# Kernel tuning notes

Measured on AMD Instinct MI355X. Metric: run time of the kernel, lower is better.

The kernel has to match this reference:

```python
import jax, jax.numpy as jnp
import numpy as np

B, T = 64, 2000
Q_DIM, MEM_DIM, ATT_DIM = 1024, 512, 128
N_FILTERS, KERNEL = 32, 31


def setup_inputs() -> dict:
    key = jax.random.key(0)
    ks = jax.random.split(key, 8)
    s = lambda fan_in: 1.0 / np.sqrt(fan_in)
    return {
        "attention_hidden_state": jax.random.normal(ks[0], (B, Q_DIM), jnp.float32),
        "memory": jax.random.normal(ks[1], (B, T, MEM_DIM), jnp.float32),
        "attention_weights_cat": jax.random.uniform(ks[2], (B, 2, T), jnp.float32),
        "W_query": jax.random.normal(ks[3], (Q_DIM, ATT_DIM), jnp.float32) * s(Q_DIM),
        "W_memory": jax.random.normal(ks[4], (MEM_DIM, ATT_DIM), jnp.float32) * s(MEM_DIM),
        "W_v": jax.random.normal(ks[5], (ATT_DIM, 1), jnp.float32) * s(ATT_DIM),
        "W_conv": jax.random.normal(ks[6], (KERNEL, 2, N_FILTERS), jnp.float32) * s(KERNEL * 2),  # WIO layout
        "W_loc": jax.random.normal(ks[7], (N_FILTERS, ATT_DIM), jnp.float32) * s(N_FILTERS),
    }


def reference(attention_hidden_state, memory, attention_weights_cat,
              W_query, W_memory, W_v, W_conv, W_loc):
    # processed query: [B, 1, D]
    pq = jnp.tanh(attention_hidden_state @ W_query)[:, None, :]
    # processed memory: [B, T, D]
    pm = jnp.tanh(jnp.einsum('btm,md->btd', memory, W_memory))
    # location features: Conv1D 'same', no bias, channels-last input [B, T, 2]
    awc = jnp.transpose(attention_weights_cat, (0, 2, 1))
    conv = jax.lax.conv_general_dilated(
        awc, W_conv, window_strides=(1,), padding='SAME',
        dimension_numbers=('NWC', 'WIO', 'NWC'))  # [B, T, F]
    ploc = jnp.tanh(conv @ W_loc)  # [B, T, D]
    # energies: [B, T]
    energies = jnp.squeeze(jnp.tanh(pq + ploc + pm) @ W_v, -1)
    attention_weights = jax.nn.softmax(energies, axis=1)  # [B, T]
    attention_context = jnp.einsum('bt,btm->bm', attention_weights, memory)
    return attention_context, attention_weights
```

## Files before the change

kernel.cpp:

```cpp
#include <hip/hip_runtime.h>
#include <hip/hip_bf16.h>

typedef __attribute__((ext_vector_type(8))) short s16x8;
typedef __attribute__((ext_vector_type(4))) float f32x4;

#define B_SZ 64
#define T_SZ 2000
#define QD 1024
#define MD 512
#define AD 128
#define NF 32
#define KW 31
#define TT 64
#define NT2 32
#define ASTRIDE 1056

__device__ __forceinline__ unsigned short f2bf(float f) {
    unsigned int u = __float_as_uint(f);
    unsigned int r = (u + 0x7FFFu + ((u >> 16) & 1u)) >> 16;
    return (unsigned short)r;
}
__device__ __forceinline__ unsigned int pack2bf_manual(float a, float b) {
    return (unsigned int)f2bf(a) | ((unsigned int)f2bf(b) << 16);
}
__device__ __forceinline__ unsigned int pack2bf(float a, float b) {
    union { __hip_bfloat162 h; unsigned int u; } cv;
    cv.h = __float22bfloat162_rn(float2{a, b});
    return cv.u;
}
__device__ __forceinline__ float fast_tanh(float x) {
    float ax = fabsf(x);
    float e = __expf(2.0f * ax);
    float r = 1.0f - 2.0f * __builtin_amdgcn_rcpf(e + 1.0f);
    return x < 0.0f ? -r : r;
}

__global__ __launch_bounds__(256) void prep_kernel(
    const float* __restrict__ ahs, const float* __restrict__ Wq,
    const float* __restrict__ Wm, const float* __restrict__ Wl,
    float* __restrict__ pq, unsigned short* __restrict__ WB,
    unsigned short* __restrict__ WL) {
    const int blk = blockIdx.x, tid = threadIdx.x;
    if (blk < 64) {
        __shared__ float q_sm[QD];
        __shared__ float part[AD];
        ((float4*)q_sm)[tid] = ((const float4*)(ahs + blk * QD))[tid];
        __syncthreads();
        const int d = tid & 127, kh = tid >> 7;
        const int k0 = kh * 512;
        float a0 = 0, a1 = 0, a2 = 0, a3 = 0;
        for (int k = k0; k < k0 + 512; k += 4) {
            a0 += q_sm[k]     * Wq[(k)     * AD + d];
            a1 += q_sm[k + 1] * Wq[(k + 1) * AD + d];
            a2 += q_sm[k + 2] * Wq[(k + 2) * AD + d];
            a3 += q_sm[k + 3] * Wq[(k + 3) * AD + d];
        }
        float s = (a0 + a1) + (a2 + a3);
        if (kh) part[d] = s;
        __syncthreads();
        if (tid < AD) pq[blk * AD + tid] = fast_tanh(s + part[tid]);
    } else if (blk < 96) {
        int cidx = (blk - 64) * 256 + tid;
        int n = cidx >> 10, s = (cidx >> 6) & 15, l = cidx & 63;
        int col = n * 16 + (l & 15);
        int krow = s * 32 + (l >> 4) * 8;
        float v[8];
        #pragma unroll
        for (int j = 0; j < 8; ++j) v[j] = Wm[(krow + j) * AD + col];
        uint4 pk;
        pk.x = pack2bf(v[0], v[1]); pk.y = pack2bf(v[2], v[3]);
        pk.z = pack2bf(v[4], v[5]); pk.w = pack2bf(v[6], v[7]);
        *(uint4*)(WB + cidx * 8) = pk;
    } else {
        for (int h = 0; h < 2; ++h) {
            int cidx = h * 256 + tid;
            int n = cidx >> 6, l = cidx & 63;
            int col = n * 16 + (l & 15);
            int krow = (l >> 4) * 8;
            float v[8];
            #pragma unroll
            for (int j = 0; j < 8; ++j) v[j] = Wl[(krow + j) * AD + col];
            uint4 pk;
            pk.x = pack2bf_manual(v[0], v[1]); pk.y = pack2bf_manual(v[2], v[3]);
            pk.z = pack2bf_manual(v[4], v[5]); pk.w = pack2bf_manual(v[6], v[7]);
            *(uint4*)(WL + cidx * 8) = pk;
        }
    }
}

__global__ __launch_bounds__(512, 4) void energy_kernel(
    const float* __restrict__ memory, const float* __restrict__ awcat,
    const float* __restrict__ Wconv, const float* __restrict__ Wv,
    const float* __restrict__ pq, const unsigned short* __restrict__ WB,
    const unsigned short* __restrict__ WL, float* __restrict__ wts,
    float* __restrict__ ctile, float* __restrict__ mloc,
    float* __restrict__ Stile) {
    const int tile = blockIdx.x;
    const int b = blockIdx.y;
    const int t0 = tile * TT;
    const int tid = threadIdx.x;

    __shared__ __align__(16) unsigned short Atile[TT * (ASTRIDE / 2)];
    __shared__ float aw_sm[2][96];
    __shared__ __align__(16) unsigned short conv_sm[TT * 40];
    __shared__ float e_part[TT][8];
    __shared__ float e_sm[TT];
    __shared__ float p_sm[TT];
    __shared__ float cpart[2][MD];

    if (tid < 192) {
        int c = tid / 96, i = tid % 96;
        float v = 0.0f;
        int tv = t0 - 15 + i;
        if (i < 94 && tv >= 0 && tv < T_SZ) v = awcat[(b * 2 + c) * T_SZ + tv];
        aw_sm[c][i] = v;
    }

    {
        const float4* msrc = (const float4*)(memory + ((size_t)b * T_SZ + t0) * MD);
        #pragma unroll
        for (int it = 0; it < 8; ++it) {
            int cid = it * 512 + tid;
            int r = cid >> 6, cc = cid & 63;
            float4 v0 = {0, 0, 0, 0}, v1 = {0, 0, 0, 0};
            if (t0 + r < T_SZ) {
                v0 = msrc[r * 128 + cc * 2];
                v1 = msrc[r * 128 + cc * 2 + 1];
            }
            uint4 pk;
            pk.x = pack2bf(v0.x, v0.y); pk.y = pack2bf(v0.z, v0.w);
            pk.z = pack2bf(v1.x, v1.y); pk.w = pack2bf(v1.z, v1.w);
            int off = r * ASTRIDE + ((cc * 16) ^ ((r & 7) << 4));
            *(uint4*)((char*)Atile + off) = pk;
        }
    }
    __syncthreads();

    {
        int f = tid & 31, tq = tid >> 5;
        float acc[4] = {0, 0, 0, 0};
        for (int k = 0; k < KW; ++k) {
            #pragma unroll
            for (int c = 0; c < 2; ++c) {
                float wv = Wconv[(k * 2 + c) * NF + f];
                #pragma unroll
                for (int tt = 0; tt < 4; ++tt)
                    acc[tt] += wv * aw_sm[c][tq + tt * 16 + k];
            }
        }
        #pragma unroll
        for (int tt = 0; tt < 4; ++tt)
            conv_sm[(tq + tt * 16) * 40 + f] = f2bf(acc[tt]);
    }
    __syncthreads();

    const int w = tid >> 6, l = tid & 63;
    const int lr = l & 15, lg = l >> 4;
    const int d = w * 16 + lr;
    const float pqv = pq[b * AD + d];
    const float wvv = Wv[d];

    f32x4 zero4 = {0, 0, 0, 0};
    f32x4 acc[4] = {zero4, zero4, zero4, zero4};

    const s16x8* wbp = (const s16x8*)WB;
    const int swz = (lr & 7) << 4;
    const char* Ac = (const char*)Atile;

    #pragma unroll
    for (int s = 0; s < 16; ++s) {
        s16x8 bf = wbp[(w * 16 + s) * 64 + l];
        int j = (lg * 16 + s * 64) ^ swz;
        #pragma unroll
        for (int rt = 0; rt < 4; ++rt) {
            s16x8 a = *(const s16x8*)(Ac + (rt * 16 + lr) * ASTRIDE + j);
            acc[rt] = __builtin_amdgcn_mfma_f32_16x16x32_bf16(a, bf, acc[rt], 0, 0, 0);
        }
    }

    const s16x8* wlp = (const s16x8*)WL;
    s16x8 lb = wlp[w * 64 + l];
    f32x4 q[4];
    #pragma unroll
    for (int rt = 0; rt < 4; ++rt) {
        s16x8 la = *(const s16x8*)((const char*)conv_sm + ((rt * 16 + lr) * 80 + lg * 16));
        q[rt] = __builtin_amdgcn_mfma_f32_16x16x32_bf16(la, lb, zero4, 0, 0, 0);
    }

    #pragma unroll
    for (int rt = 0; rt < 4; ++rt) {
        #pragma unroll
        for (int r = 0; r < 4; ++r) {
            float v = fast_tanh(pqv + fast_tanh(q[rt][r]) + fast_tanh(acc[rt][r])) * wvv;
            v += __shfl_xor(v, 1);
            v += __shfl_xor(v, 2);
            v += __shfl_xor(v, 4);
            v += __shfl_xor(v, 8);
            if (lr == 0) e_part[rt * 16 + lg * 4 + r][w] = v;
        }
    }
    __syncthreads();

    {
        int t = tid >> 3, g = tid & 7;
        float v = e_part[t][g];
        v += __shfl_xor(v, 1);
        v += __shfl_xor(v, 2);
        v += __shfl_xor(v, 4);
        if (g == 0) e_sm[t] = (t0 + t < T_SZ) ? v : -3.4e38f;
    }
    __syncthreads();

    if (tid < TT) {
        float e = e_sm[tid];
        float m = e;
        m = fmaxf(m, __shfl_xor(m, 1));  m = fmaxf(m, __shfl_xor(m, 2));
        m = fmaxf(m, __shfl_xor(m, 4));  m = fmaxf(m, __shfl_xor(m, 8));
        m = fmaxf(m, __shfl_xor(m, 16)); m = fmaxf(m, __shfl_xor(m, 32));
        bool valid = (t0 + tid < T_SZ);
        float p = valid ? __expf(e - m) : 0.0f;
        p_sm[tid] = p;
        float S = p;
        S += __shfl_xor(S, 1);  S += __shfl_xor(S, 2);
        S += __shfl_xor(S, 4);  S += __shfl_xor(S, 8);
        S += __shfl_xor(S, 16); S += __shfl_xor(S, 32);
        if (valid) wts[b * T_SZ + t0 + tid] = p;
        if (tid == 0) { mloc[b * NT2 + tile] = m; Stile[b * NT2 + tile] = S; }
    }
    __syncthreads();

    {
        int grp = tid >> 8, idx = tid & 255;
        int boff = idx * 4;
        float c0 = 0.0f, c1 = 0.0f;
        #pragma unroll
        for (int tt = 0; tt < 32; ++tt) {
            int t = grp * 32 + tt;
            float p = p_sm[t];
            unsigned int pk = *(const unsigned int*)(
                Ac + t * ASTRIDE + (boff ^ ((t & 7) << 4)));
            c0 += p * __uint_as_float(pk << 16);
            c1 += p * __uint_as_float(pk & 0xffff0000u);
        }
        cpart[grp][idx * 2]     = c0;
        cpart[grp][idx * 2 + 1] = c1;
    }
    __syncthreads();
    ctile[((b * NT2 + tile) << 9) + tid] = cpart[0][tid] + cpart[1][tid];
}

__global__ __launch_bounds__(256) void finalize_kernel(
    const float* __restrict__ mloc, const float* __restrict__ Stile,
    const float* __restrict__ ctile, float* __restrict__ wts,
    float* __restrict__ ctx) {
    const int b = blockIdx.x, h = blockIdx.y, tid = threadIdx.x;
    __shared__ float sc_sm[NT2];
    if (tid < 64) {
        float m = (tid < NT2) ? mloc[b * NT2 + tid] : -3.4e38f;
        float s = (tid < NT2) ? Stile[b * NT2 + tid] : 0.0f;
        float M = m;
        M = fmaxf(M, __shfl_xor(M, 1));  M = fmaxf(M, __shfl_xor(M, 2));
        M = fmaxf(M, __shfl_xor(M, 4));  M = fmaxf(M, __shfl_xor(M, 8));
        M = fmaxf(M, __shfl_xor(M, 16)); M = fmaxf(M, __shfl_xor(M, 32));
        float e = __expf(m - M);
        float z = e * s;
        z += __shfl_xor(z, 1);  z += __shfl_xor(z, 2);
        z += __shfl_xor(z, 4);  z += __shfl_xor(z, 8);
        z += __shfl_xor(z, 16); z += __shfl_xor(z, 32);
        if (tid < NT2) sc_sm[tid] = e / z;
    }
    __syncthreads();

    if (h == 0) {
        #pragma unroll
        for (int i = 0; i < 8; ++i) {
            int idx = tid + i * 256;
            if (idx < T_SZ) wts[b * T_SZ + idx] *= sc_sm[idx >> 6];
        }
    }

    float a = 0.0f;
    const float* cb = ctile + ((size_t)b * NT2 << 9) + h * 256 + tid;
    #pragma unroll 8
    for (int tl = 0; tl < NT2; ++tl) a += sc_sm[tl] * cb[tl << 9];
    ctx[b * MD + h * 256 + tid] = a;
}

extern "C" void kernel_launch(void* const* d_in, const int* in_sizes, int n_in,
                              void* d_out, int out_size, void* d_ws, size_t ws_size,
                              hipStream_t stream) {
    const float* ahs    = (const float*)d_in[0];
    const float* memory = (const float*)d_in[1];
    const float* awcat  = (const float*)d_in[2];
    const float* Wq     = (const float*)d_in[3];
    const float* Wm     = (const float*)d_in[4];
    const float* Wv     = (const float*)d_in[5];
    const float* Wconv  = (const float*)d_in[6];
    const float* Wl     = (const float*)d_in[7];

    float* out = (float*)d_out;
    float* ctx = out;
    float* wts = out + B_SZ * MD;

    char* ws = (char*)d_ws;
    float* pq             = (float*)(ws);
    unsigned short* WB    = (unsigned short*)(ws + 32768);
    unsigned short* WL    = (unsigned short*)(ws + 163840);
    float* mloc           = (float*)(ws + 172032);
    float* Stile          = (float*)(ws + 180224);
    float* ctile          = (float*)(ws + 196608);

    prep_kernel<<<97, 256, 0, stream>>>(ahs, Wq, Wm, Wl, pq, WB, WL);
    energy_kernel<<<dim3(NT2, B_SZ), 512, 0, stream>>>(
        memory, awcat, Wconv, Wv, pq, WB, WL, wts, ctile, mloc, Stile);
    finalize_kernel<<<dim3(B_SZ, 2), 256, 0, stream>>>(mloc, Stile, ctile, wts, ctx);
}
```

Measured before the change: 100.3 us.

## Halve energy tile to 32 timesteps with 2x2 MFMA register blocking per wave

```diff
diff --git a/kernel.cpp b/kernel.cpp
--- a/kernel.cpp
+++ b/kernel.cpp
@@ -11,8 +11,7 @@
 #define AD 128
 #define NF 32
 #define KW 31
-#define TT 64
-#define NT2 32
+#define NTILE 63
 #define ASTRIDE 1056
 
 __device__ __forceinline__ unsigned short f2bf(float f) {
@@ -35,7 +34,7 @@
     return x < 0.0f ? -r : r;
 }
 
-__global__ __launch_bounds__(256) void prep_kernel(
+__global__ __launch_bounds__(512) void prep_kernel(
     const float* __restrict__ ahs, const float* __restrict__ Wq,
     const float* __restrict__ Wm, const float* __restrict__ Wl,
     float* __restrict__ pq, unsigned short* __restrict__ WB,
@@ -43,24 +42,27 @@
     const int blk = blockIdx.x, tid = threadIdx.x;
     if (blk < 64) {
         __shared__ float q_sm[QD];
-        __shared__ float part[AD];
-        ((float4*)q_sm)[tid] = ((const float4*)(ahs + blk * QD))[tid];
+        __shared__ float part[3][AD];
+        ((float2*)q_sm)[tid] = ((const float2*)(ahs + blk * QD))[tid];
         __syncthreads();
         const int d = tid & 127, kh = tid >> 7;
-        const int k0 = kh * 512;
+        const int k0 = kh * 256;
         float a0 = 0, a1 = 0, a2 = 0, a3 = 0;
-        for (int k = k0; k < k0 + 512; k += 4) {
+        #pragma unroll 4
+        for (int k = k0; k < k0 + 256; k += 4) {
             a0 += q_sm[k]     * Wq[(k)     * AD + d];
             a1 += q_sm[k + 1] * Wq[(k + 1) * AD + d];
             a2 += q_sm[k + 2] * Wq[(k + 2) * AD + d];
             a3 += q_sm[k + 3] * Wq[(k + 3) * AD + d];
         }
         float s = (a0 + a1) + (a2 + a3);
-        if (kh) part[d] = s;
+        if (kh) part[kh - 1][d] = s;
         __syncthreads();
-        if (tid < AD) pq[blk * AD + tid] = fast_tanh(s + part[tid]);
-    } else if (blk < 96) {
-        int cidx = (blk - 64) * 256 + tid;
+        if (tid < AD)
+            pq[blk * AD + tid] =
+                fast_tanh((s + part[0][tid]) + (part[1][tid] + part[2][tid]));
+    } else if (blk < 80) {
+        int cidx = (blk - 64) * 512 + tid;
         int n = cidx >> 10, s = (cidx >> 6) & 15, l = cidx & 63;
         int col = n * 16 + (l & 15);
         int krow = s * 32 + (l >> 4) * 8;
@@ -72,23 +74,21 @@
         pk.z = pack2bf(v[4], v[5]); pk.w = pack2bf(v[6], v[7]);
         *(uint4*)(WB + cidx * 8) = pk;
     } else {
-        for (int h = 0; h < 2; ++h) {
-            int cidx = h * 256 + tid;
-            int n = cidx >> 6, l = cidx & 63;
-            int col = n * 16 + (l & 15);
-            int krow = (l >> 4) * 8;
-            float v[8];
-            #pragma unroll
-            for (int j = 0; j < 8; ++j) v[j] = Wl[(krow + j) * AD + col];
-            uint4 pk;
-            pk.x = pack2bf_manual(v[0], v[1]); pk.y = pack2bf_manual(v[2], v[3]);
-            pk.z = pack2bf_manual(v[4], v[5]); pk.w = pack2bf_manual(v[6], v[7]);
-            *(uint4*)(WL + cidx * 8) = pk;
-        }
-    }
-}
-
-__global__ __launch_bounds__(512, 4) void energy_kernel(
+        int cidx = tid;
+        int n = cidx >> 6, l = cidx & 63;
+        int col = n * 16 + (l & 15);
+        int krow = (l >> 4) * 8;
+        float v[8];
+        #pragma unroll
+        for (int j = 0; j < 8; ++j) v[j] = Wl[(krow + j) * AD + col];
+        uint4 pk;
+        pk.x = pack2bf_manual(v[0], v[1]); pk.y = pack2bf_manual(v[2], v[3]);
+        pk.z = pack2bf_manual(v[4], v[5]); pk.w = pack2bf_manual(v[6], v[7]);
+        *(uint4*)(WL + cidx * 8) = pk;
+    }
+}
+
+__global__ __launch_bounds__(256) void energy_kernel(
     const float* __restrict__ memory, const float* __restrict__ awcat,
     const float* __restrict__ Wconv, const float* __restrict__ Wv,
     const float* __restrict__ pq, const unsigned short* __restrict__ WB,
@@ -97,22 +97,20 @@
     float* __restrict__ Stile) {
     const int tile = blockIdx.x;
     const int b = blockIdx.y;
-    const int t0 = tile * TT;
+    const int t0 = tile * 32;
     const int tid = threadIdx.x;
 
-    __shared__ __align__(16) unsigned short Atile[TT * (ASTRIDE / 2)];
-    __shared__ float aw_sm[2][96];
-    __shared__ __align__(16) unsigned short conv_sm[TT * 40];
-    __shared__ float e_part[TT][8];
-    __shared__ float e_sm[TT];
-    __shared__ float p_sm[TT];
-    __shared__ float cpart[2][MD];
-
-    if (tid < 192) {
-        int c = tid / 96, i = tid % 96;
+    __shared__ __align__(16) unsigned short Atile[32 * (ASTRIDE / 2)];
+    __shared__ float aw_sm[2][64];
+    __shared__ __align__(16) unsigned short conv_sm[32 * 40];
+    __shared__ float e_part[32][4];
+    __shared__ float p_sm[32];
+
+    if (tid < 128) {
+        int c = tid >> 6, i = tid & 63;
         float v = 0.0f;
         int tv = t0 - 15 + i;
-        if (i < 94 && tv >= 0 && tv < T_SZ) v = awcat[(b * 2 + c) * T_SZ + tv];
+        if (i < 63 && tv >= 0 && tv < T_SZ) v = awcat[(b * 2 + c) * T_SZ + tv];
         aw_sm[c][i] = v;
     }
 
@@ -120,7 +118,7 @@
         const float4* msrc = (const float4*)(memory + ((size_t)b * T_SZ + t0) * MD);
         #pragma unroll
         for (int it = 0; it < 8; ++it) {
-            int cid = it * 512 + tid;
+            int cid = it * 256 + tid;
             int r = cid >> 6, cc = cid & 63;
             float4 v0 = {0, 0, 0, 0}, v1 = {0, 0, 0, 0};
             if (t0 + r < T_SZ) {
@@ -145,108 +143,110 @@
                 float wv = Wconv[(k * 2 + c) * NF + f];
                 #pragma unroll
                 for (int tt = 0; tt < 4; ++tt)
-                    acc[tt] += wv * aw_sm[c][tq + tt * 16 + k];
+                    acc[tt] += wv * aw_sm[c][tq + tt * 8 + k];
             }
         }
         #pragma unroll
         for (int tt = 0; tt < 4; ++tt)
-            conv_sm[(tq + tt * 16) * 40 + f] = f2bf(acc[tt]);
+            conv_sm[(tq + tt * 8) * 40 + f] = f2bf(acc[tt]);
     }
     __syncthreads();
 
     const int w = tid >> 6, l = tid & 63;
     const int lr = l & 15, lg = l >> 4;
-    const int d = w * 16 + lr;
-    const float pqv = pq[b * AD + d];
-    const float wvv = Wv[d];
+    const int d0 = (2 * w + 0) * 16 + lr;
+    const int d1 = (2 * w + 1) * 16 + lr;
+    const float pqv0 = pq[b * AD + d0], pqv1 = pq[b * AD + d1];
+    const float wvv0 = Wv[d0], wvv1 = Wv[d1];
 
     f32x4 zero4 = {0, 0, 0, 0};
-    f32x4 acc[4] = {zero4, zero4, zero4, zero4};
+    f32x4 p00 = zero4, p01 = zero4, p10 = zero4, p11 = zero4;
 
     const s16x8* wbp = (const s16x8*)WB;
     const int swz = (lr & 7) << 4;
-    const char* Ac = (const char*)Atile;
+    const int rbase0 = lr * ASTRIDE;
+    const int rbase1 = (16 + lr) * ASTRIDE;
+    const int inb = lg * 16;
 
     #pragma unroll
     for (int s = 0; s < 16; ++s) {
-        s16x8 bf = wbp[(w * 16 + s) * 64 + l];
-        int j = (lg * 16 + s * 64) ^ swz;
-        #pragma unroll
-        for (int rt = 0; rt < 4; ++rt) {
-            s16x8 a = *(const s16x8*)(Ac + (rt * 16 + lr) * ASTRIDE + j);
-            acc[rt] = __builtin_amdgcn_mfma_f32_16x16x32_bf16(a, bf, acc[rt], 0, 0, 0);
-        }
-    }
-
+        int j = (inb + s * 64) ^ swz;
+        s16x8 a0 = *(const s16x8*)((const char*)Atile + rbase0 + j);
+        s16x8 a1 = *(const s16x8*)((const char*)Atile + rbase1 + j);
+        s16x8 b0 = wbp[((2 * w + 0) * 16 + s) * 64 + l];
+        s16x8 b1 = wbp[((2 * w + 1) * 16 + s) * 64 + l];
+        p00 = __builtin_amdgcn_mfma_f32_16x16x32_bf16(a0, b0, p00, 0, 0, 0);
+        p01 = __builtin_amdgcn_mfma_f32_16x16x32_bf16(a0, b1, p01, 0, 0, 0);
+        p10 = __builtin_amdgcn_mfma_f32_16x16x32_bf16(a1, b0, p10, 0, 0, 0);
+        p11 = __builtin_amdgcn_mfma_f32_16x16x32_bf16(a1, b1, p11, 0, 0, 0);
+    }
+
+    s16x8 la0 = *(const s16x8*)((const char*)conv_sm + (lr * 80 + lg * 16));
+    s16x8 la1 = *(const s16x8*)((const char*)conv_sm + ((16 + lr) * 80 + lg * 16));
     const s16x8* wlp = (const s16x8*)WL;
-    s16x8 lb = wlp[w * 64 + l];
-    f32x4 q[4];
+    s16x8 lb0 = wlp[(2 * w + 0) * 64 + l];
+    s16x8 lb1 = wlp[(2 * w + 1) * 64 + l];
+    f32x4 q00 = __builtin_amdgcn_mfma_f32_16x16x32_bf16(la0, lb0, zero4, 0, 0, 0);
+    f32x4 q01 = __builtin_amdgcn_mfma_f32_16x16x32_bf16(la0, lb1, zero4, 0, 0, 0);
+    f32x4 q10 = __builtin_amdgcn_mfma_f32_16x16x32_bf16(la1, lb0, zero4, 0, 0, 0);
+    f32x4 q11 = __builtin_amdgcn_mfma_f32_16x16x32_bf16(la1, lb1, zero4, 0, 0, 0);
+
+    float vr[8];
     #pragma unroll
-    for (int rt = 0; rt < 4; ++rt) {
-        s16x8 la = *(const s16x8*)((const char*)conv_sm + ((rt * 16 + lr) * 80 + lg * 16));
-        q[rt] = __builtin_amdgcn_mfma_f32_16x16x32_bf16(la, lb, zero4, 0, 0, 0);
-    }
-
+    for (int r = 0; r < 4; ++r) {
+        vr[r]     = fast_tanh(pqv0 + fast_tanh(q00[r]) + fast_tanh(p00[r])) * wvv0
+                  + fast_tanh(pqv1 + fast_tanh(q01[r]) + fast_tanh(p01[r])) * wvv1;
+        vr[4 + r] = fast_tanh(pqv0 + fast_tanh(q10[r]) + fast_tanh(p10[r])) * wvv0
+                  + fast_tanh(pqv1 + fast_tanh(q11[r]) + fast_tanh(p11[r])) * wvv1;
+    }
     #pragma unroll
-    for (int rt = 0; rt < 4; ++rt) {
-        #pragma unroll
-        for (int r = 0; r < 4; ++r) {
-            float v = fast_tanh(pqv + fast_tanh(q[rt][r]) + fast_tanh(acc[rt][r])) * wvv;
-            v += __shfl_xor(v, 1);
-            v += __shfl_xor(v, 2);
-            v += __shfl_xor(v, 4);
-            v += __shfl_xor(v, 8);
-            if (lr == 0) e_part[rt * 16 + lg * 4 + r][w] = v;
-        }
-    }
-    __syncthreads();
-
-    {
-        int t = tid >> 3, g = tid & 7;
-        float v = e_part[t][g];
+    for (int j = 0; j < 8; ++j) {
+        float v = vr[j];
         v += __shfl_xor(v, 1);
         v += __shfl_xor(v, 2);
         v += __shfl_xor(v, 4);
-        if (g == 0) e_sm[t] = (t0 + t < T_SZ) ? v : -3.4e38f;
-    }
-    __syncthreads();
-
-    if (tid < TT) {
-        float e = e_sm[tid];
-        float m = e;
-        m = fmaxf(m, __shfl_xor(m, 1));  m = fmaxf(m, __shfl_xor(m, 2));
-        m = fmaxf(m, __shfl_xor(m, 4));  m = fmaxf(m, __shfl_xor(m, 8));
-        m = fmaxf(m, __shfl_xor(m, 16)); m = fmaxf(m, __shfl_xor(m, 32));
-        bool valid = (t0 + tid < T_SZ);
+        v += __shfl_xor(v, 8);
+        if (lr == 0) e_part[(j >> 2) * 16 + lg * 4 + (j & 3)][w] = v;
+    }
+    __syncthreads();
+
+    if (tid < 32) {
+        int t = t0 + tid;
+        bool valid = t < T_SZ;
+        float e = (e_part[tid][0] + e_part[tid][1]) + (e_part[tid][2] + e_part[tid][3]);
+        float m = valid ? e : -3.4e38f;
+        m = fmaxf(m, __shfl_xor(m, 1));
+        m = fmaxf(m, __shfl_xor(m, 2));
+        m = fmaxf(m, __shfl_xor(m, 4));
+        m = fmaxf(m, __shfl_xor(m, 8));
+        m = fmaxf(m, __shfl_xor(m, 16));
         float p = valid ? __expf(e - m) : 0.0f;
         p_sm[tid] = p;
         float S = p;
-        S += __shfl_xor(S, 1);  S += __shfl_xor(S, 2);
-        S += __shfl_xor(S, 4);  S += __shfl_xor(S, 8);
-        S += __shfl_xor(S, 16); S += __shfl_xor(S, 32);
-        if (valid) wts[b * T_SZ + t0 + tid] = p;
-        if (tid == 0) { mloc[b * NT2 + tile] = m; Stile[b * NT2 + tile] = S; }
+        S += __shfl_xor(S, 1);
+        S += __shfl_xor(S, 2);
+        S += __shfl_xor(S, 4);
+        S += __shfl_xor(S, 8);
+        S += __shfl_xor(S, 16);
+        if (valid) wts[b * T_SZ + t] = p;
+        if (tid == 0) { mloc[b * NTILE + tile] = m; Stile[b * NTILE + tile] = S; }
     }
     __syncthreads();
 
     {
-        int grp = tid >> 8, idx = tid & 255;
-        int boff = idx * 4;
         float c0 = 0.0f, c1 = 0.0f;
-        #pragma unroll
-        for (int tt = 0; tt < 32; ++tt) {
-            int t = grp * 32 + tt;
+        const int boff = tid * 4;
+        #pragma unroll
+        for (int t = 0; t < 32; ++t) {
             float p = p_sm[t];
             unsigned int pk = *(const unsigned int*)(
-                Ac + t * ASTRIDE + (boff ^ ((t & 7) << 4)));
+                (const char*)Atile + t * ASTRIDE + (boff ^ ((t & 7) << 4)));
             c0 += p * __uint_as_float(pk << 16);
             c1 += p * __uint_as_float(pk & 0xffff0000u);
         }
-        cpart[grp][idx * 2]     = c0;
-        cpart[grp][idx * 2 + 1] = c1;
-    }
-    __syncthreads();
-    ctile[((b * NT2 + tile) << 9) + tid] = cpart[0][tid] + cpart[1][tid];
+        float2 o; o.x = c0; o.y = c1;
+        ((float2*)ctile)[((b * NTILE + tile) << 8) + tid] = o;
+    }
 }
 
 __global__ __launch_bounds__(256) void finalize_kernel(
@@ -254,10 +254,10 @@
     const float* __restrict__ ctile, float* __restrict__ wts,
     float* __restrict__ ctx) {
     const int b = blockIdx.x, h = blockIdx.y, tid = threadIdx.x;
-    __shared__ float sc_sm[NT2];
+    __shared__ float sc_sm[NTILE + 1];
     if (tid < 64) {
-        float m = (tid < NT2) ? mloc[b * NT2 + tid] : -3.4e38f;
-        float s = (tid < NT2) ? Stile[b * NT2 + tid] : 0.0f;
+        float m = (tid < NTILE) ? mloc[b * NTILE + tid] : -3.4e38f;
+        float s = (tid < NTILE) ? Stile[b * NTILE + tid] : 0.0f;
         float M = m;
         M = fmaxf(M, __shfl_xor(M, 1));  M = fmaxf(M, __shfl_xor(M, 2));
         M = fmaxf(M, __shfl_xor(M, 4));  M = fmaxf(M, __shfl_xor(M, 8));
@@ -267,7 +267,7 @@
         z += __shfl_xor(z, 1);  z += __shfl_xor(z, 2);
         z += __shfl_xor(z, 4);  z += __shfl_xor(z, 8);
         z += __shfl_xor(z, 16); z += __shfl_xor(z, 32);
-        if (tid < NT2) sc_sm[tid] = e / z;
+        if (tid < NTILE) sc_sm[tid] = e / z;
     }
     __syncthreads();
 
@@ -275,14 +275,14 @@
         #pragma unroll
         for (int i = 0; i < 8; ++i) {
             int idx = tid + i * 256;
-            if (idx < T_SZ) wts[b * T_SZ + idx] *= sc_sm[idx >> 6];
+            if (idx < T_SZ) wts[b * T_SZ + idx] *= sc_sm[idx >> 5];
         }
     }
 
     float a = 0.0f;
-    const float* cb = ctile + ((size_t)b * NT2 << 9) + h * 256 + tid;
-    #pragma unroll 8
-    for (int tl = 0; tl < NT2; ++tl) a += sc_sm[tl] * cb[tl << 9];
+    const float* cb = ctile + ((size_t)b * NTILE << 9) + h * 256 + tid;
+    #pragma unroll 7
+    for (int tl = 0; tl < NTILE; ++tl) a += sc_sm[tl] * cb[(size_t)tl << 9];
     ctx[b * MD + h * 256 + tid] = a;
 }
 
@@ -307,11 +307,11 @@
     unsigned short* WB    = (unsigned short*)(ws + 32768);
     unsigned short* WL    = (unsigned short*)(ws + 163840);
     float* mloc           = (float*)(ws + 172032);
-    float* Stile          = (float*)(ws + 180224);
-    float* ctile          = (float*)(ws + 196608);
-
-    prep_kernel<<<97, 256, 0, stream>>>(ahs, Wq, Wm, Wl, pq, WB, WL);
-    energy_kernel<<<dim3(NT2, B_SZ), 512, 0, stream>>>(
+    float* Stile          = (float*)(ws + 188160);
+    float* ctile          = (float*)(ws + 204800);
+
+    prep_kernel<<<81, 512, 0, stream>>>(ahs, Wq, Wm, Wl, pq, WB, WL);
+    energy_kernel<<<dim3(NTILE, B_SZ), 256, 0, stream>>>(
         memory, awcat, Wconv, Wv, pq, WB, WL, wts, ctile, mloc, Stile);
     finalize_kernel<<<dim3(B_SZ, 2), 256, 0, stream>>>(mloc, Stile, ctile, wts, ctx);
 }
```

Result: faster. 91.40 us (-8.9%).
